# Performance work log

Measured on AMD Instinct MI355X. Metric: run time of the kernel, lower is better.

## Reference

```python
import jax, jax.numpy as jnp
import numpy as np
from jax import lax

N_FFT = 1024
HOP = 64
SR = 16000
N_MELS = 80
N_ITER = 300
N_FRAMES = 512
N_BINS = N_FFT // 2 + 1  # 513
SIG_LEN = N_FFT + HOP * (N_FRAMES - 1)  # 33728 (center=False istft length)

# periodic hann window (librosa default, sym=False)
_WIN_NP = (0.5 - 0.5 * np.cos(2.0 * np.pi * np.arange(N_FFT) / N_FFT)).astype(np.float32)
_WIN = jnp.asarray(_WIN_NP)
# frame gather indices for center=False framing: [N_FRAMES, N_FFT]
_FRAME_IDX_NP = np.arange(N_FRAMES)[:, None] * HOP + np.arange(N_FFT)[None, :]
_FRAME_IDX = jnp.asarray(_FRAME_IDX_NP)
# window-sum-squares normalization for istft overlap-add
_wss = np.zeros(SIG_LEN, np.float32)
np.add.at(_wss, _FRAME_IDX_NP, np.broadcast_to(_WIN_NP**2, (N_FRAMES, N_FFT)))
_WSS_SAFE = jnp.asarray(np.where(_wss > 1e-11, _wss, 1.0).astype(np.float32))


def _mel_filterbank(sr, n_fft, n_mels, fmin=0.0, fmax=None):
    """librosa.filters.mel with defaults: slaney mel scale, slaney norm."""
    if fmax is None:
        fmax = sr / 2.0
    f_sp = 200.0 / 3.0
    min_log_hz = 1000.0
    min_log_mel = min_log_hz / f_sp
    logstep = np.log(6.4) / 27.0

    def hz2mel(f):
        f = np.asarray(f, dtype=np.float64)
        return np.where(f >= min_log_hz,
                        min_log_mel + np.log(np.maximum(f, min_log_hz) / min_log_hz) / logstep,
                        f / f_sp)

    def mel2hz(m):
        m = np.asarray(m, dtype=np.float64)
        return np.where(m >= min_log_mel,
                        min_log_hz * np.exp(logstep * (m - min_log_mel)),
                        m * f_sp)

    mel_f = mel2hz(np.linspace(hz2mel(fmin), hz2mel(fmax), n_mels + 2))
    fft_f = np.linspace(0.0, sr / 2.0, 1 + n_fft // 2)
    fdiff = np.diff(mel_f)
    ramps = mel_f[:, None] - fft_f[None, :]
    lower = -ramps[:-2] / fdiff[:-1, None]
    upper = ramps[2:] / fdiff[1:, None]
    weights = np.maximum(0.0, np.minimum(lower, upper))
    enorm = 2.0 / (mel_f[2:n_mels + 2] - mel_f[:n_mels])  # slaney norm
    weights *= enorm[:, None]
    return weights.astype(np.float32)  # [n_mels, n_bins]


def _stft(x):
    # x: [SIG_LEN] -> [N_BINS, N_FRAMES], center=False, hann window
    frames = x[_FRAME_IDX] * _WIN  # [N_FRAMES, N_FFT]
    return jnp.fft.rfft(frames, axis=-1).T


def _istft(S):
    # S: [N_BINS, N_FRAMES] -> [SIG_LEN], center=False, hann window, NOLA norm
    frames = jnp.fft.irfft(S.T, n=N_FFT, axis=-1) * _WIN  # [N_FRAMES, N_FFT]
    ola = jnp.zeros(SIG_LEN, dtype=frames.dtype).at[_FRAME_IDX].add(frames)
    return ola / _WSS_SAFE


def setup_inputs() -> dict:
    key = jax.random.key(0)
    mel = jax.random.normal(key, (N_MELS, N_FRAMES), dtype=jnp.float32)
    basis = _mel_filterbank(SR, N_FFT, N_MELS)           # [80, 513]
    inv_mel_basis = np.linalg.pinv(basis).astype(np.float32)  # [513, 80]
    return {"mel": mel, "inv_mel_basis": jnp.asarray(inv_mel_basis)}


def reference(mel, inv_mel_basis):
    # mel -> linear magnitude via pseudo-inverse mel basis
    mag = inv_mel_basis @ jnp.power(10.0, mel)  # [N_BINS, N_FRAMES]

    def step(X_best, _):
        x_t = _istft(X_best)
        est = _stft(x_t)
        phase = est / jnp.maximum(1e-8, jnp.abs(est))
        return (mag * phase).astype(jnp.complex64), None

    X0 = mag.astype(jnp.complex64)
    X_final, _ = lax.scan(step, X0, None, length=N_ITER)
    return jnp.real(_istft(X_final))  # [SIG_LEN]
```

## Files before the change

kernel.cpp:

```cpp
#include <hip/hip_runtime.h>
#include <math.h>

#define NFFT   1024
#define NH     512
#define HOP    64
#define NMELS  80
#define NFR    512
#define NBINS  513
#define NITER  300
#define SIGLEN 33728
#define NSEG   527
#define NT     256
#define NB     512

#define TBL_WIN  0
#define TBL_TWR  1024
#define TBL_TWI  1280
#define TBL_W1R  1536
#define TBL_W1I  2056
#define BAR_SLOT 2624
#define BAR_GEN  3200
#define OFF_MAG  4096
#define OFF_IWS  266752
#define OFF_F    300480
#define OFF_X    824768

typedef unsigned long long u64;
typedef unsigned int u32;

__device__ __forceinline__ float4 coh_load4(const float* p) {
    u64 a = __hip_atomic_load((const u64*)p,       __ATOMIC_RELAXED, __HIP_MEMORY_SCOPE_AGENT);
    u64 b = __hip_atomic_load((const u64*)(p + 2), __ATOMIC_RELAXED, __HIP_MEMORY_SCOPE_AGENT);
    float2 fa, fb;
    __builtin_memcpy(&fa, &a, 8);
    __builtin_memcpy(&fb, &b, 8);
    return make_float4(fa.x, fa.y, fb.x, fb.y);
}
__device__ __forceinline__ void coh_store4(float* p, float4 v) {
    float2 fa = make_float2(v.x, v.y), fb = make_float2(v.z, v.w);
    u64 a, b;
    __builtin_memcpy(&a, &fa, 8);
    __builtin_memcpy(&b, &fb, 8);
    __hip_atomic_store((u64*)p,       a, __ATOMIC_RELAXED, __HIP_MEMORY_SCOPE_AGENT);
    __hip_atomic_store((u64*)(p + 2), b, __ATOMIC_RELAXED, __HIP_MEMORY_SCOPE_AGENT);
}
__device__ __forceinline__ float coh_load1(const float* p) {
    u32 a = __hip_atomic_load((const u32*)p, __ATOMIC_RELAXED, __HIP_MEMORY_SCOPE_AGENT);
    float f;
    __builtin_memcpy(&f, &a, 4);
    return f;
}
__device__ __forceinline__ void coh_store1(float* p, float v) {
    u32 a;
    __builtin_memcpy(&a, &v, 4);
    __hip_atomic_store((u32*)p, a, __ATOMIC_RELAXED, __HIP_MEMORY_SCOPE_AGENT);
}

template<int P, int SH, bool INV>
__device__ __forceinline__ void r4b(const float* __restrict__ sR, const float* __restrict__ sI,
                                    float* __restrict__ dR, float* __restrict__ dI,
                                    const float* twr, const float* twi, int j) {
    int k  = j & (P - 1);
    int d0 = ((j - k) << 2) + k;
    float x0r = sR[j],       x0i = sI[j];
    float x1r = sR[j + 128], x1i = sI[j + 128];
    float x2r = sR[j + 256], x2i = sI[j + 256];
    float x3r = sR[j + 384], x3i = sI[j + 384];
    int tb = k << SH;
    float c1 = twr[tb], s1 = twi[tb];
    if (INV) s1 = -s1;
    float c2 = c1 * c1 - s1 * s1, s2 = 2.f * c1 * s1;
    float c3 = c1 * c2 - s1 * s2, s3 = c1 * s2 + s1 * c2;
    float a1r = x1r * c1 - x1i * s1, a1i = x1r * s1 + x1i * c1;
    float a2r = x2r * c2 - x2i * s2, a2i = x2r * s2 + x2i * c2;
    float a3r = x3r * c3 - x3i * s3, a3i = x3r * s3 + x3i * c3;
    float t0r = x0r + a2r, t0i = x0i + a2i;
    float t1r = x0r - a2r, t1i = x0i - a2i;
    float t2r = a1r + a3r, t2i = a1i + a3i;
    float t3r = a1r - a3r, t3i = a1i - a3i;
    float i3r = INV ? -t3i : t3i;
    float i3i = INV ?  t3r : -t3r;
    dR[d0]         = t0r + t2r;  dI[d0]         = t0i + t2i;
    dR[d0 + P]     = t1r + i3r;  dI[d0 + P]     = t1i + i3i;
    dR[d0 + 2 * P] = t0r - t2r;  dI[d0 + 2 * P] = t0i - t2i;
    dR[d0 + 3 * P] = t1r - i3r;  dI[d0 + 3 * P] = t1i - i3i;
}

struct __align__(16) SMemI {
    float xb[NFFT];
    float C0r[NH], C0i[NH];
    float C1r[NH], C1i[NH];
    float win[NFFT];
    float twr[256], twi[256];
    float mag[516];
};

extern "C" __global__ __launch_bounds__(NT)
void k_init(const float* __restrict__ mel,
            const float* __restrict__ invmel,
            float* __restrict__ ws) {
    __shared__ SMemI sm;
    const int tid = threadIdx.x;
    const int t   = blockIdx.x;

    for (int n = tid; n < NFFT; n += NT) {
        double a = (2.0 * 3.14159265358979323846) * (double)n / 1024.0;
        sm.win[n] = (float)(0.5 - 0.5 * cos(a));
    }
    for (int j = tid; j < 256; j += NT) {
        double a = (2.0 * 3.14159265358979323846) * (double)j / 512.0;
        sm.twr[j] = (float)cos(a);
        sm.twi[j] = (float)(-sin(a));
    }
    __syncthreads();
    if (t == 0) {
        for (int n = tid; n < NFFT; n += NT) ws[TBL_WIN + n] = sm.win[n];
        for (int j = tid; j < 256; j += NT) {
            ws[TBL_TWR + j] = sm.twr[j];
            ws[TBL_TWI + j] = sm.twi[j];
        }
        for (int k = tid; k < NBINS; k += NT) {
            double a = (2.0 * 3.14159265358979323846) * (double)k / 1024.0;
            ws[TBL_W1R + k] = (float)cos(a);
            ws[TBL_W1I + k] = (float)sin(a);
        }
        ((int*)ws)[BAR_SLOT + tid]       = 0;
        ((int*)ws)[BAR_SLOT + 256 + tid] = 0;
        if (tid == 0) ((int*)ws)[BAR_GEN] = 0;
    }

    for (int p = t * NT + tid; p < SIGLEN; p += NFR * NT) {
        int tq = p >> 6, io = p & 63;
        float s = 0.f;
#pragma unroll
        for (int m = 0; m < 16; ++m) {
            int tp = tq - m;
            if (tp >= 0 && tp < NFR) {
                float w = sm.win[io + (m << 6)];
                s += w * w;
            }
        }
        ws[OFF_IWS + p] = (s > 1e-11f) ? (1.0f / s) : 1.0f;
    }

    if (tid < NMELS) sm.xb[tid] = exp10f(mel[tid * NFR + t]);
    __syncthreads();
    for (int k = tid; k < NBINS; k += NT) {
        const float* row = invmel + k * NMELS;
        float s = 0.f;
#pragma unroll 8
        for (int j = 0; j < NMELS; ++j) s += row[j] * sm.xb[j];
        ws[OFF_MAG + t * NBINS + k] = s;
        sm.mag[k] = s;
    }
    __syncthreads();

    for (int k = tid; k < NH; k += NT) {
        float xr = sm.mag[k], yr = sm.mag[512 - k];
        double a = (2.0 * 3.14159265358979323846) * (double)k / 1024.0;
        float c = (float)cos(a), s = (float)sin(a);
        float dr = xr - yr;
        sm.C1r[k] = ((xr + yr) - s * dr) * (1.0f / 1024.0f);
        sm.C1i[k] = (c * dr) * (1.0f / 1024.0f);
    }
    __syncthreads();
    if (tid < 128) {
        float x0r = sm.C1r[tid],       x0i = sm.C1i[tid];
        float x1r = sm.C1r[tid + 128], x1i = sm.C1i[tid + 128];
        float x2r = sm.C1r[tid + 256], x2i = sm.C1i[tid + 256];
        float x3r = sm.C1r[tid + 384], x3i = sm.C1i[tid + 384];
        float t0r = x0r + x2r, t0i = x0i + x2i;
        float t1r = x0r - x2r, t1i = x0i - x2i;
        float t2r = x1r + x3r, t2i = x1i + x3i;
        float t3r = x1r - x3r, t3i = x1i - x3i;
        float4 vr = make_float4(t0r + t2r, t1r - t3i, t0r - t2r, t1r + t3i);
        float4 vi = make_float4(t0i + t2i, t1i + t3r, t0i - t2i, t1i - t3r);
        ((float4*)sm.C0r)[tid] = vr;
        ((float4*)sm.C0i)[tid] = vi;
    }
    __syncthreads();
    if (tid < 128) r4b<4, 5, true>(sm.C0r, sm.C0i, sm.C1r, sm.C1i, sm.twr, sm.twi, tid);
    __syncthreads();
    if (tid < 128) r4b<16, 3, true>(sm.C1r, sm.C1i, sm.C0r, sm.C0i, sm.twr, sm.twi, tid);
    __syncthreads();
    if (tid < 128) r4b<64, 1, true>(sm.C0r, sm.C0i, sm.C1r, sm.C1i, sm.twr, sm.twi, tid);
    __syncthreads();
    {
        float c = sm.twr[tid], s = -sm.twi[tid];
        float x0r = sm.C1r[tid], x0i = sm.C1i[tid];
        float x1r = sm.C1r[tid + 256], x1i = sm.C1i[tid + 256];
        float ar = x1r * c - x1i * s, ai = x1r * s + x1i * c;
        sm.C0r[tid]       = x0r + ar;  sm.C0i[tid]       = x0i + ai;
        sm.C0r[tid + 256] = x0r - ar;  sm.C0i[tid + 256] = x0i - ai;
    }
    __syncthreads();

    float4 w4 = ((float4*)sm.win)[tid];
    float4 o;
    o.x = w4.x * sm.C0r[2 * tid];
    o.y = w4.y * sm.C0i[2 * tid];
    o.z = w4.z * sm.C0r[2 * tid + 1];
    o.w = w4.w * sm.C0i[2 * tid + 1];
    *(float4*)&ws[OFF_F + (t << 10) + (tid << 2)] = o;
}

struct __align__(16) SM1 {
    float C0r[NH], C0i[NH];
    float C1r[NH], C1i[NH];
    float twr[256], twi[256];
};

__device__ __forceinline__ void gbar(int* bar, int t, int tid, int bc) {
    __syncthreads();
    if (tid == 0)
        __hip_atomic_store(bar + BAR_SLOT + t, bc,
                           __ATOMIC_RELAXED, __HIP_MEMORY_SCOPE_AGENT);
    if (t == 0) {
        while (__hip_atomic_load(bar + BAR_SLOT + tid,
                                 __ATOMIC_RELAXED, __HIP_MEMORY_SCOPE_AGENT) < bc)
            __builtin_amdgcn_s_sleep(1);
        while (__hip_atomic_load(bar + BAR_SLOT + 256 + tid,
                                 __ATOMIC_RELAXED, __HIP_MEMORY_SCOPE_AGENT) < bc)
            __builtin_amdgcn_s_sleep(1);
        __syncthreads();
        if (tid == 0)
            __hip_atomic_store(bar + BAR_GEN, bc,
                               __ATOMIC_RELAXED, __HIP_MEMORY_SCOPE_AGENT);
    }
    if (tid == 0) {
        while (__hip_atomic_load(bar + BAR_GEN,
                                 __ATOMIC_RELAXED, __HIP_MEMORY_SCOPE_AGENT) < bc)
            __builtin_amdgcn_s_sleep(2);
    }
    __syncthreads();
}

extern "C" __global__ __launch_bounds__(NT)
void k_persist(float* __restrict__ ws, float* __restrict__ out) {
    __shared__ SM1 sm;
    const int tid = threadIdx.x;
    const int t   = blockIdx.x;
    const int i0  = tid << 2;
    const int j2  = 512 - tid;
    const int n0  = tid << 1;

    const float* tbl  = ws;
    const float* magg = ws + OFF_MAG;
    const float* iws  = ws + OFF_IWS;
    float* F  = ws + OFF_F;
    float* X  = ws + OFF_X;
    int*   bar = (int*)ws;

    if (tid < 64)       ((float4*)sm.twr)[tid]      = ((const float4*)(tbl + TBL_TWR))[tid];
    else if (tid < 128) ((float4*)sm.twi)[tid - 64] = ((const float4*)(tbl + TBL_TWI))[tid - 64];

    float4 w4 = ((const float4*)(tbl + TBL_WIN))[tid];
    float m_a, m_b, m_ny = 0.f, w1r_a, w1i_a, w1r_b, w1i_b;
    {
        const int s0 = t * NBINS;
        if (tid == 0) {
            m_a = magg[s0]; m_ny = magg[s0 + 512]; m_b = magg[s0 + 256];
            w1r_a = 1.f; w1i_a = 0.f; w1r_b = 0.f; w1i_b = 1.f;
        } else {
            m_a = magg[s0 + tid]; m_b = magg[s0 + j2];
            w1r_a = tbl[TBL_W1R + tid]; w1i_a = tbl[TBL_W1I + tid];
            w1r_b = tbl[TBL_W1R + j2];  w1i_b = tbl[TBL_W1I + j2];
        }
    }
    const bool extra = (t >= 497);
    int gseg = -1;
    if (tid < 64) gseg = t;
    else if (tid < 128 && extra) gseg = t + 15;
    const int u = tid & 63;
    float iwreg = 0.f;
    if (gseg >= 0) iwreg = iws[(gseg << 6) + u];

    if (gseg >= 0) {
        float acc = 0.f;
#pragma unroll
        for (int m = 0; m < 16; ++m) {
            int tp = gseg - m;
            if (tp >= 0 && tp < NFR)
                acc += coh_load1(&F[(tp << 10) + u + (m << 6)]);
        }
        coh_store1(&X[(gseg << 6) + u], acc * iwreg);
    }
    gbar(bar, t, tid, 1);

    int bc = 2;
#pragma unroll 1
    for (int it = 1; it <= NITER; ++it) {
        {
            float4 xv = coh_load4(&X[(t << 6) + i0]);
            sm.C1r[n0]     = xv.x * w4.x;
            sm.C1i[n0]     = xv.y * w4.y;
            sm.C1r[n0 + 1] = xv.z * w4.z;
            sm.C1i[n0 + 1] = xv.w * w4.w;
        }
        __syncthreads();
        if (tid < 128) {
            float x0r = sm.C1r[tid],       x0i = sm.C1i[tid];
            float x1r = sm.C1r[tid + 128], x1i = sm.C1i[tid + 128];
            float x2r = sm.C1r[tid + 256], x2i = sm.C1i[tid + 256];
            float x3r = sm.C1r[tid + 384], x3i = sm.C1i[tid + 384];
            float t0r = x0r + x2r, t0i = x0i + x2i;
            float t1r = x0r - x2r, t1i = x0i - x2i;
            float t2r = x1r + x3r, t2i = x1i + x3i;
            float t3r = x1r - x3r, t3i = x1i - x3i;
            float4 vr = make_float4(t0r + t2r, t1r + t3i, t0r - t2r, t1r - t3i);
            float4 vi = make_float4(t0i + t2i, t1i - t3r, t0i - t2i, t1i + t3r);
            ((float4*)sm.C0r)[tid] = vr;
            ((float4*)sm.C0i)[tid] = vi;
        }
        __syncthreads();
        if (tid < 128) r4b<4, 5, false>(sm.C0r, sm.C0i, sm.C1r, sm.C1i, sm.twr, sm.twi, tid);
        __syncthreads();
        if (tid < 128) r4b<16, 3, false>(sm.C1r, sm.C1i, sm.C0r, sm.C0i, sm.twr, sm.twi, tid);
        __syncthreads();
        if (tid < 128) r4b<64, 1, false>(sm.C0r, sm.C0i, sm.C1r, sm.C1i, sm.twr, sm.twi, tid);
        __syncthreads();
        {
            float c = sm.twr[tid], s = sm.twi[tid];
            float x0r = sm.C1r[tid], x0i = sm.C1i[tid];
            float x1r = sm.C1r[tid + 256], x1i = sm.C1i[tid + 256];
            float ar = x1r * c - x1i * s, ai = x1r * s + x1i * c;
            sm.C0r[tid]       = x0r + ar;  sm.C0i[tid]       = x0i + ai;
            sm.C0r[tid + 256] = x0r - ar;  sm.C0i[tid + 256] = x0i - ai;
        }
        __syncthreads();

        if (tid == 0) {
            float zr = sm.C0r[0], zi = sm.C0i[0];
            float e0 = zr + zi;
            float e5 = zr - zi;
            float X0 = m_a  * e0 / fmaxf(1e-8f, fabsf(e0));
            float X5 = m_ny * e5 / fmaxf(1e-8f, fabsf(e5));
            sm.C1r[0] = (X0 + X5) * (1.0f / 1024.0f);
            sm.C1i[0] = (X0 - X5) * (1.0f / 1024.0f);
            float z6r = sm.C0r[256], z6i = sm.C0i[256];
            float sc6 = m_b / fmaxf(1e-8f, sqrtf(z6r * z6r + z6i * z6i));
            float X6r = z6r * sc6, X6i = -z6i * sc6;
            sm.C1r[256] = X6r * (2.0f / 1024.0f);
            sm.C1i[256] = -X6i * (2.0f / 1024.0f);
        } else {
            float zr = sm.C0r[tid], zi = sm.C0i[tid];
            float ur = sm.C0r[j2],  ui = sm.C0i[j2];
            float er = 0.5f * (zr + ur), ei = 0.5f * (zi - ui);
            float dr = zr - ur,          di = zi + ui;
            float odr = 0.5f * di, odi = -0.5f * dr;
            float e1r = er + w1r_a * odr + w1i_a * odi;
            float e1i = ei + w1r_a * odi - w1i_a * odr;
            float e2r =  er + w1r_b * odr - w1i_b * odi;
            float e2i = -ei - w1r_b * odi - w1i_b * odr;
            float sc1 = m_a / fmaxf(1e-8f, sqrtf(e1r * e1r + e1i * e1i));
            float sc2 = m_b / fmaxf(1e-8f, sqrtf(e2r * e2r + e2i * e2i));
            float X1r = e1r * sc1, X1i = e1i * sc1;
            float X2r = e2r * sc2, X2i = e2i * sc2;
            float Er = X1r + X2r, Ei = X1i - X2i;
            float Dr = X1r - X2r, Di = X1i + X2i;
            float wdr = w1r_a * Dr - w1i_a * Di, wdi = w1r_a * Di + w1i_a * Dr;
            sm.C1r[tid] = (Er - wdi) * (1.0f / 1024.0f);
            sm.C1i[tid] = (Ei + wdr) * (1.0f / 1024.0f);
            float wdr2 = -w1r_b * Dr - w1i_b * Di, wdi2 = w1r_b * Di - w1i_b * Dr;
            sm.C1r[j2] = (Er - wdi2) * (1.0f / 1024.0f);
            sm.C1i[j2] = (-Ei + wdr2) * (1.0f / 1024.0f);
        }
        __syncthreads();

        if (tid < 128) {
            float x0r = sm.C1r[tid],       x0i = sm.C1i[tid];
            float x1r = sm.C1r[tid + 128], x1i = sm.C1i[tid + 128];
            float x2r = sm.C1r[tid + 256], x2i = sm.C1i[tid + 256];
            float x3r = sm.C1r[tid + 384], x3i = sm.C1i[tid + 384];
            float t0r = x0r + x2r, t0i = x0i + x2i;
            float t1r = x0r - x2r, t1i = x0i - x2i;
            float t2r = x1r + x3r, t2i = x1i + x3i;
            float t3r = x1r - x3r, t3i = x1i - x3i;
            float4 vr = make_float4(t0r + t2r, t1r - t3i, t0r - t2r, t1r + t3i);
            float4 vi = make_float4(t0i + t2i, t1i + t3r, t0i - t2i, t1i - t3r);
            ((float4*)sm.C0r)[tid] = vr;
            ((float4*)sm.C0i)[tid] = vi;
        }
        __syncthreads();
        if (tid < 128) r4b<4, 5, true>(sm.C0r, sm.C0i, sm.C1r, sm.C1i, sm.twr, sm.twi, tid);
        __syncthreads();
        if (tid < 128) r4b<16, 3, true>(sm.C1r, sm.C1i, sm.C0r, sm.C0i, sm.twr, sm.twi, tid);
        __syncthreads();
        if (tid < 128) r4b<64, 1, true>(sm.C0r, sm.C0i, sm.C1r, sm.C1i, sm.twr, sm.twi, tid);
        __syncthreads();
        {
            float c = sm.twr[tid], s = -sm.twi[tid];
            float x0r = sm.C1r[tid], x0i = sm.C1i[tid];
            float x1r = sm.C1r[tid + 256], x1i = sm.C1i[tid + 256];
            float ar = x1r * c - x1i * s, ai = x1r * s + x1i * c;
            sm.C0r[tid]       = x0r + ar;  sm.C0i[tid]       = x0i + ai;
            sm.C0r[tid + 256] = x0r - ar;  sm.C0i[tid + 256] = x0i - ai;
        }
        __syncthreads();

        {
            float4 o;
            o.x = w4.x * sm.C0r[n0];
            o.y = w4.y * sm.C0i[n0];
            o.z = w4.z * sm.C0r[n0 + 1];
            o.w = w4.w * sm.C0i[n0 + 1];
            coh_store4(&F[(t << 10) + i0], o);
        }
        gbar(bar, t, tid, bc++);

        if (gseg >= 0) {
            float acc = 0.f;
#pragma unroll
            for (int m = 0; m < 16; ++m) {
                int tp = gseg - m;
                if (tp >= 0 && tp < NFR)
                    acc += coh_load1(&F[(tp << 10) + u + (m << 6)]);
            }
            float val = acc * iwreg;
            if (it < NITER) coh_store1(&X[(gseg << 6) + u], val);
            else            out[(gseg << 6) + u] = val;
        }
        if (it < NITER)
            gbar(bar, t, tid, bc++);
    }
}

extern "C" void kernel_launch(void* const* d_in, const int* in_sizes, int n_in,
                              void* d_out, int out_size, void* d_ws, size_t ws_size,
                              hipStream_t stream) {
    const float* mel    = (const float*)d_in[0];
    const float* invmel = (const float*)d_in[1];
    float* out = (float*)d_out;
    float* ws  = (float*)d_ws;

    k_init<<<NFR, NT, 0, stream>>>(mel, invmel, ws);
    k_persist<<<NB, NT, 0, stream>>>(ws, out);
}
```

Before: 3.108 ms.

## Shrink persistent blocks to a single wavefront and vectorize barrier polling

Each persistent block (one per frame) now runs one 64-lane wavefront instead of 256 threads. Every lane processes several FFT elements per stage, and window, magnitude and twiddle tables are staged in shared memory instead of registers. With one wave per block, __syncthreads becomes nearly free, and the grid barrier's master block polls 8 slots per lane across 64 lanes rather than 256 lanes in two passes. The aim is to cut intra-block and grid-barrier synchronisation cost in the 300-iteration loop. In exchange, each wave does four times the serial work per FFT stage, with more LDS traffic and fewer threads to hide latency.

```diff
diff --git a/kernel.cpp b/kernel.cpp
--- a/kernel.cpp
+++ b/kernel.cpp
@@ -9,8 +9,8 @@
 #define NBINS  513
 #define NITER  300
 #define SIGLEN 33728
-#define NSEG   527
-#define NT     256
+#define NTI    256
+#define NTW    64
 #define NB     512
 
 #define TBL_WIN  0
@@ -95,7 +95,7 @@
     float mag[516];
 };
 
-extern "C" __global__ __launch_bounds__(NT)
+extern "C" __global__ __launch_bounds__(NTI)
 void k_init(const float* __restrict__ mel,
             const float* __restrict__ invmel,
             float* __restrict__ ws) {
@@ -103,23 +103,23 @@
     const int tid = threadIdx.x;
     const int t   = blockIdx.x;
 
-    for (int n = tid; n < NFFT; n += NT) {
+    for (int n = tid; n < NFFT; n += NTI) {
         double a = (2.0 * 3.14159265358979323846) * (double)n / 1024.0;
         sm.win[n] = (float)(0.5 - 0.5 * cos(a));
     }
-    for (int j = tid; j < 256; j += NT) {
+    for (int j = tid; j < 256; j += NTI) {
         double a = (2.0 * 3.14159265358979323846) * (double)j / 512.0;
         sm.twr[j] = (float)cos(a);
         sm.twi[j] = (float)(-sin(a));
     }
     __syncthreads();
     if (t == 0) {
-        for (int n = tid; n < NFFT; n += NT) ws[TBL_WIN + n] = sm.win[n];
-        for (int j = tid; j < 256; j += NT) {
+        for (int n = tid; n < NFFT; n += NTI) ws[TBL_WIN + n] = sm.win[n];
+        for (int j = tid; j < 256; j += NTI) {
             ws[TBL_TWR + j] = sm.twr[j];
             ws[TBL_TWI + j] = sm.twi[j];
         }
-        for (int k = tid; k < NBINS; k += NT) {
+        for (int k = tid; k < NBINS; k += NTI) {
             double a = (2.0 * 3.14159265358979323846) * (double)k / 1024.0;
             ws[TBL_W1R + k] = (float)cos(a);
             ws[TBL_W1I + k] = (float)sin(a);
@@ -129,7 +129,7 @@
         if (tid == 0) ((int*)ws)[BAR_GEN] = 0;
     }
 
-    for (int p = t * NT + tid; p < SIGLEN; p += NFR * NT) {
+    for (int p = t * NTI + tid; p < SIGLEN; p += NFR * NTI) {
         int tq = p >> 6, io = p & 63;
         float s = 0.f;
 #pragma unroll
@@ -145,7 +145,7 @@
 
     if (tid < NMELS) sm.xb[tid] = exp10f(mel[tid * NFR + t]);
     __syncthreads();
-    for (int k = tid; k < NBINS; k += NT) {
+    for (int k = tid; k < NBINS; k += NTI) {
         const float* row = invmel + k * NMELS;
         float s = 0.f;
 #pragma unroll 8
@@ -155,7 +155,7 @@
     }
     __syncthreads();
 
-    for (int k = tid; k < NH; k += NT) {
+    for (int k = tid; k < NH; k += NTI) {
         float xr = sm.mag[k], yr = sm.mag[512 - k];
         double a = (2.0 * 3.14159265358979323846) * (double)k / 1024.0;
         float c = (float)cos(a), s = (float)sin(a);
@@ -204,30 +204,46 @@
     *(float4*)&ws[OFF_F + (t << 10) + (tid << 2)] = o;
 }
 
-struct __align__(16) SM1 {
+struct __align__(16) SMW {
     float C0r[NH], C0i[NH];
     float C1r[NH], C1i[NH];
     float twr[256], twi[256];
+    float win[NFFT];
+    float mag[520], w1r[520], w1i[520];
 };
 
-__device__ __forceinline__ void gbar(int* bar, int t, int tid, int bc) {
-    __syncthreads();
-    if (tid == 0)
+__device__ __forceinline__ void gbar(int* bar, int t, int l, int bc) {
+    __syncthreads();
+    if (l == 0)
         __hip_atomic_store(bar + BAR_SLOT + t, bc,
                            __ATOMIC_RELAXED, __HIP_MEMORY_SCOPE_AGENT);
     if (t == 0) {
-        while (__hip_atomic_load(bar + BAR_SLOT + tid,
-                                 __ATOMIC_RELAXED, __HIP_MEMORY_SCOPE_AGENT) < bc)
+        const int* base = bar + BAR_SLOT + (l << 3);
+        for (;;) {
+            int a0 = __hip_atomic_load(base + 0, __ATOMIC_RELAXED, __HIP_MEMORY_SCOPE_AGENT);
+            int a1 = __hip_atomic_load(base + 1, __ATOMIC_RELAXED, __HIP_MEMORY_SCOPE_AGENT);
+            int a2 = __hip_atomic_load(base + 2, __ATOMIC_RELAXED, __HIP_MEMORY_SCOPE_AGENT);
+            int a3 = __hip_atomic_load(base + 3, __ATOMIC_RELAXED, __HIP_MEMORY_SCOPE_AGENT);
+            int a4 = __hip_atomic_load(base + 4, __ATOMIC_RELAXED, __HIP_MEMORY_SCOPE_AGENT);
+            int a5 = __hip_atomic_load(base + 5, __ATOMIC_RELAXED, __HIP_MEMORY_SCOPE_AGENT);
+            int a6 = __hip_atomic_load(base + 6, __ATOMIC_RELAXED, __HIP_MEMORY_SCOPE_AGENT);
+            int a7 = __hip_atomic_load(base + 7, __ATOMIC_RELAXED, __HIP_MEMORY_SCOPE_AGENT);
+            int m01 = a0 < a1 ? a0 : a1;
+            int m23 = a2 < a3 ? a2 : a3;
+            int m45 = a4 < a5 ? a4 : a5;
+            int m67 = a6 < a7 ? a6 : a7;
+            int m03 = m01 < m23 ? m01 : m23;
+            int m47 = m45 < m67 ? m45 : m67;
+            int mn  = m03 < m47 ? m03 : m47;
+            if (mn >= bc) break;
             __builtin_amdgcn_s_sleep(1);
-        while (__hip_atomic_load(bar + BAR_SLOT + 256 + tid,
-                                 __ATOMIC_RELAXED, __HIP_MEMORY_SCOPE_AGENT) < bc)
-            __builtin_amdgcn_s_sleep(1);
-        __syncthreads();
-        if (tid == 0)
+        }
+        __syncthreads();
+        if (l == 0)
             __hip_atomic_store(bar + BAR_GEN, bc,
                                __ATOMIC_RELAXED, __HIP_MEMORY_SCOPE_AGENT);
     }
-    if (tid == 0) {
+    if (l == 0) {
         while (__hip_atomic_load(bar + BAR_GEN,
                                  __ATOMIC_RELAXED, __HIP_MEMORY_SCOPE_AGENT) < bc)
             __builtin_amdgcn_s_sleep(2);
@@ -235,14 +251,11 @@
     __syncthreads();
 }
 
-extern "C" __global__ __launch_bounds__(NT)
+extern "C" __global__ __launch_bounds__(NTW)
 void k_persist(float* __restrict__ ws, float* __restrict__ out) {
-    __shared__ SM1 sm;
-    const int tid = threadIdx.x;
-    const int t   = blockIdx.x;
-    const int i0  = tid << 2;
-    const int j2  = 512 - tid;
-    const int n0  = tid << 1;
+    __shared__ SMW sm;
+    const int l = threadIdx.x;
+    const int t = blockIdx.x;
 
     const float* tbl  = ws;
     const float* magg = ws + OFF_MAG;
@@ -251,177 +264,220 @@
     float* X  = ws + OFF_X;
     int*   bar = (int*)ws;
 
-    if (tid < 64)       ((float4*)sm.twr)[tid]      = ((const float4*)(tbl + TBL_TWR))[tid];
-    else if (tid < 128) ((float4*)sm.twi)[tid - 64] = ((const float4*)(tbl + TBL_TWI))[tid - 64];
-
-    float4 w4 = ((const float4*)(tbl + TBL_WIN))[tid];
-    float m_a, m_b, m_ny = 0.f, w1r_a, w1i_a, w1r_b, w1i_b;
+    ((float4*)sm.twr)[l] = ((const float4*)(tbl + TBL_TWR))[l];
+    ((float4*)sm.twi)[l] = ((const float4*)(tbl + TBL_TWI))[l];
+#pragma unroll
+    for (int c = 0; c < 4; ++c)
+        ((float4*)sm.win)[l + (c << 6)] = ((const float4*)(tbl + TBL_WIN))[l + (c << 6)];
+    for (int k = l; k < NBINS; k += NTW) {
+        sm.mag[k] = magg[t * NBINS + k];
+        sm.w1r[k] = tbl[TBL_W1R + k];
+        sm.w1i[k] = tbl[TBL_W1I + k];
+    }
+    const bool extra = (t >= 497);
+    float iw0 = iws[(t << 6) + l];
+    float iw1 = extra ? iws[((t + 15) << 6) + l] : 0.f;
+    __syncthreads();
+
     {
-        const int s0 = t * NBINS;
-        if (tid == 0) {
-            m_a = magg[s0]; m_ny = magg[s0 + 512]; m_b = magg[s0 + 256];
-            w1r_a = 1.f; w1i_a = 0.f; w1r_b = 0.f; w1i_b = 1.f;
-        } else {
-            m_a = magg[s0 + tid]; m_b = magg[s0 + j2];
-            w1r_a = tbl[TBL_W1R + tid]; w1i_a = tbl[TBL_W1I + tid];
-            w1r_b = tbl[TBL_W1R + j2];  w1i_b = tbl[TBL_W1I + j2];
-        }
-    }
-    const bool extra = (t >= 497);
-    int gseg = -1;
-    if (tid < 64) gseg = t;
-    else if (tid < 128 && extra) gseg = t + 15;
-    const int u = tid & 63;
-    float iwreg = 0.f;
-    if (gseg >= 0) iwreg = iws[(gseg << 6) + u];
-
-    if (gseg >= 0) {
         float acc = 0.f;
 #pragma unroll
         for (int m = 0; m < 16; ++m) {
-            int tp = gseg - m;
+            int tp = t - m;
             if (tp >= 0 && tp < NFR)
-                acc += coh_load1(&F[(tp << 10) + u + (m << 6)]);
-        }
-        coh_store1(&X[(gseg << 6) + u], acc * iwreg);
-    }
-    gbar(bar, t, tid, 1);
+                acc += coh_load1(&F[(tp << 10) + l + (m << 6)]);
+        }
+        coh_store1(&X[(t << 6) + l], acc * iw0);
+        if (extra) {
+            int g = t + 15;
+            float acc2 = 0.f;
+#pragma unroll
+            for (int m = 0; m < 16; ++m) {
+                int tp = g - m;
+                if (tp >= 0 && tp < NFR)
+                    acc2 += coh_load1(&F[(tp << 10) + l + (m << 6)]);
+            }
+            coh_store1(&X[(g << 6) + l], acc2 * iw1);
+        }
+    }
+    gbar(bar, t, l, 1);
 
     int bc = 2;
 #pragma unroll 1
     for (int it = 1; it <= NITER; ++it) {
-        {
+#pragma unroll
+        for (int c = 0; c < 4; ++c) {
+            int tp = l + (c << 6);
+            int i0 = tp << 2;
             float4 xv = coh_load4(&X[(t << 6) + i0]);
-            sm.C1r[n0]     = xv.x * w4.x;
-            sm.C1i[n0]     = xv.y * w4.y;
-            sm.C1r[n0 + 1] = xv.z * w4.z;
-            sm.C1i[n0 + 1] = xv.w * w4.w;
-        }
-        __syncthreads();
-        if (tid < 128) {
-            float x0r = sm.C1r[tid],       x0i = sm.C1i[tid];
-            float x1r = sm.C1r[tid + 128], x1i = sm.C1i[tid + 128];
-            float x2r = sm.C1r[tid + 256], x2i = sm.C1i[tid + 256];
-            float x3r = sm.C1r[tid + 384], x3i = sm.C1i[tid + 384];
+            float4 wv = ((float4*)sm.win)[tp];
+            int n0 = tp << 1;
+            sm.C1r[n0]     = xv.x * wv.x;
+            sm.C1i[n0]     = xv.y * wv.y;
+            sm.C1r[n0 + 1] = xv.z * wv.z;
+            sm.C1i[n0 + 1] = xv.w * wv.w;
+        }
+        __syncthreads();
+#pragma unroll
+        for (int c = 0; c < 2; ++c) {
+            int j = l + (c << 6);
+            float x0r = sm.C1r[j],       x0i = sm.C1i[j];
+            float x1r = sm.C1r[j + 128], x1i = sm.C1i[j + 128];
+            float x2r = sm.C1r[j + 256], x2i = sm.C1i[j + 256];
+            float x3r = sm.C1r[j + 384], x3i = sm.C1i[j + 384];
             float t0r = x0r + x2r, t0i = x0i + x2i;
             float t1r = x0r - x2r, t1i = x0i - x2i;
             float t2r = x1r + x3r, t2i = x1i + x3i;
             float t3r = x1r - x3r, t3i = x1i - x3i;
             float4 vr = make_float4(t0r + t2r, t1r + t3i, t0r - t2r, t1r - t3i);
             float4 vi = make_float4(t0i + t2i, t1i - t3r, t0i - t2i, t1i + t3r);
-            ((float4*)sm.C0r)[tid] = vr;
-            ((float4*)sm.C0i)[tid] = vi;
-        }
-        __syncthreads();
-        if (tid < 128) r4b<4, 5, false>(sm.C0r, sm.C0i, sm.C1r, sm.C1i, sm.twr, sm.twi, tid);
-        __syncthreads();
-        if (tid < 128) r4b<16, 3, false>(sm.C1r, sm.C1i, sm.C0r, sm.C0i, sm.twr, sm.twi, tid);
-        __syncthreads();
-        if (tid < 128) r4b<64, 1, false>(sm.C0r, sm.C0i, sm.C1r, sm.C1i, sm.twr, sm.twi, tid);
-        __syncthreads();
-        {
-            float c = sm.twr[tid], s = sm.twi[tid];
-            float x0r = sm.C1r[tid], x0i = sm.C1i[tid];
-            float x1r = sm.C1r[tid + 256], x1i = sm.C1i[tid + 256];
-            float ar = x1r * c - x1i * s, ai = x1r * s + x1i * c;
-            sm.C0r[tid]       = x0r + ar;  sm.C0i[tid]       = x0i + ai;
-            sm.C0r[tid + 256] = x0r - ar;  sm.C0i[tid + 256] = x0i - ai;
-        }
-        __syncthreads();
-
-        if (tid == 0) {
-            float zr = sm.C0r[0], zi = sm.C0i[0];
-            float e0 = zr + zi;
-            float e5 = zr - zi;
-            float X0 = m_a  * e0 / fmaxf(1e-8f, fabsf(e0));
-            float X5 = m_ny * e5 / fmaxf(1e-8f, fabsf(e5));
-            sm.C1r[0] = (X0 + X5) * (1.0f / 1024.0f);
-            sm.C1i[0] = (X0 - X5) * (1.0f / 1024.0f);
-            float z6r = sm.C0r[256], z6i = sm.C0i[256];
-            float sc6 = m_b / fmaxf(1e-8f, sqrtf(z6r * z6r + z6i * z6i));
-            float X6r = z6r * sc6, X6i = -z6i * sc6;
-            sm.C1r[256] = X6r * (2.0f / 1024.0f);
-            sm.C1i[256] = -X6i * (2.0f / 1024.0f);
-        } else {
-            float zr = sm.C0r[tid], zi = sm.C0i[tid];
-            float ur = sm.C0r[j2],  ui = sm.C0i[j2];
-            float er = 0.5f * (zr + ur), ei = 0.5f * (zi - ui);
-            float dr = zr - ur,          di = zi + ui;
-            float odr = 0.5f * di, odi = -0.5f * dr;
-            float e1r = er + w1r_a * odr + w1i_a * odi;
-            float e1i = ei + w1r_a * odi - w1i_a * odr;
-            float e2r =  er + w1r_b * odr - w1i_b * odi;
-            float e2i = -ei - w1r_b * odi - w1i_b * odr;
-            float sc1 = m_a / fmaxf(1e-8f, sqrtf(e1r * e1r + e1i * e1i));
-            float sc2 = m_b / fmaxf(1e-8f, sqrtf(e2r * e2r + e2i * e2i));
-            float X1r = e1r * sc1, X1i = e1i * sc1;
-            float X2r = e2r * sc2, X2i = e2i * sc2;
-            float Er = X1r + X2r, Ei = X1i - X2i;
-            float Dr = X1r - X2r, Di = X1i + X2i;
-            float wdr = w1r_a * Dr - w1i_a * Di, wdi = w1r_a * Di + w1i_a * Dr;
-            sm.C1r[tid] = (Er - wdi) * (1.0f / 1024.0f);
-            sm.C1i[tid] = (Ei + wdr) * (1.0f / 1024.0f);
-            float wdr2 = -w1r_b * Dr - w1i_b * Di, wdi2 = w1r_b * Di - w1i_b * Dr;
-            sm.C1r[j2] = (Er - wdi2) * (1.0f / 1024.0f);
-            sm.C1i[j2] = (-Ei + wdr2) * (1.0f / 1024.0f);
-        }
-        __syncthreads();
-
-        if (tid < 128) {
-            float x0r = sm.C1r[tid],       x0i = sm.C1i[tid];
-            float x1r = sm.C1r[tid + 128], x1i = sm.C1i[tid + 128];
-            float x2r = sm.C1r[tid + 256], x2i = sm.C1i[tid + 256];
-            float x3r = sm.C1r[tid + 384], x3i = sm.C1i[tid + 384];
+            ((float4*)sm.C0r)[j] = vr;
+            ((float4*)sm.C0i)[j] = vi;
+        }
+        __syncthreads();
+        r4b<4, 5, false>(sm.C0r, sm.C0i, sm.C1r, sm.C1i, sm.twr, sm.twi, l);
+        r4b<4, 5, false>(sm.C0r, sm.C0i, sm.C1r, sm.C1i, sm.twr, sm.twi, l + 64);
+        __syncthreads();
+        r4b<16, 3, false>(sm.C1r, sm.C1i, sm.C0r, sm.C0i, sm.twr, sm.twi, l);
+        r4b<16, 3, false>(sm.C1r, sm.C1i, sm.C0r, sm.C0i, sm.twr, sm.twi, l + 64);
+        __syncthreads();
+        r4b<64, 1, false>(sm.C0r, sm.C0i, sm.C1r, sm.C1i, sm.twr, sm.twi, l);
+        r4b<64, 1, false>(sm.C0r, sm.C0i, sm.C1r, sm.C1i, sm.twr, sm.twi, l + 64);
+        __syncthreads();
+#pragma unroll
+        for (int c = 0; c < 4; ++c) {
+            int tp = l + (c << 6);
+            float cc = sm.twr[tp], s = sm.twi[tp];
+            float x0r = sm.C1r[tp], x0i = sm.C1i[tp];
+            float x1r = sm.C1r[tp + 256], x1i = sm.C1i[tp + 256];
+            float ar = x1r * cc - x1i * s, ai = x1r * s + x1i * cc;
+            sm.C0r[tp]       = x0r + ar;  sm.C0i[tp]       = x0i + ai;
+            sm.C0r[tp + 256] = x0r - ar;  sm.C0i[tp + 256] = x0i - ai;
+        }
+        __syncthreads();
+#pragma unroll
+        for (int c = 0; c < 4; ++c) {
+            int tp = l + (c << 6);
+            if (tp == 0) {
+                float zr = sm.C0r[0], zi = sm.C0i[0];
+                float e0 = zr + zi;
+                float e5 = zr - zi;
+                float X0 = sm.mag[0]   * e0 / fmaxf(1e-8f, fabsf(e0));
+                float X5 = sm.mag[512] * e5 / fmaxf(1e-8f, fabsf(e5));
+                sm.C1r[0] = (X0 + X5) * (1.0f / 1024.0f);
+                sm.C1i[0] = (X0 - X5) * (1.0f / 1024.0f);
+                float z6r = sm.C0r[256], z6i = sm.C0i[256];
+                float sc6 = sm.mag[256] / fmaxf(1e-8f, sqrtf(z6r * z6r + z6i * z6i));
+                float X6r = z6r * sc6, X6i = -z6i * sc6;
+                sm.C1r[256] = X6r * (2.0f / 1024.0f);
+                sm.C1i[256] = -X6i * (2.0f / 1024.0f);
+            } else {
+                int j2 = 512 - tp;
+                float m_a = sm.mag[tp], m_b = sm.mag[j2];
+                float w1r_a = sm.w1r[tp], w1i_a = sm.w1i[tp];
+                float w1r_b = sm.w1r[j2], w1i_b = sm.w1i[j2];
+                float zr = sm.C0r[tp], zi = sm.C0i[tp];
+                float ur = sm.C0r[j2], ui = sm.C0i[j2];
+                float er = 0.5f * (zr + ur), ei = 0.5f * (zi - ui);
+                float dr = zr - ur,          di = zi + ui;
+                float odr = 0.5f * di, odi = -0.5f * dr;
+                float e1r = er + w1r_a * odr + w1i_a * odi;
+                float e1i = ei + w1r_a * odi - w1i_a * odr;
+                float e2r =  er + w1r_b * odr - w1i_b * odi;
+                float e2i = -ei - w1r_b * odi - w1i_b * odr;
+                float sc1 = m_a / fmaxf(1e-8f, sqrtf(e1r * e1r + e1i * e1i));
+                float sc2 = m_b / fmaxf(1e-8f, sqrtf(e2r * e2r + e2i * e2i));
+                float X1r = e1r * sc1, X1i = e1i * sc1;
+                float X2r = e2r * sc2, X2i = e2i * sc2;
+                float Er = X1r + X2r, Ei = X1i - X2i;
+                float Dr = X1r - X2r, Di = X1i + X2i;
+                float wdr = w1r_a * Dr - w1i_a * Di, wdi = w1r_a * Di + w1i_a * Dr;
+                sm.C1r[tp] = (Er - wdi) * (1.0f / 1024.0f);
+                sm.C1i[tp] = (Ei + wdr) * (1.0f / 1024.0f);
+                float wdr2 = -w1r_b * Dr - w1i_b * Di, wdi2 = w1r_b * Di - w1i_b * Dr;
+                sm.C1r[j2] = (Er - wdi2) * (1.0f / 1024.0f);
+                sm.C1i[j2] = (-Ei + wdr2) * (1.0f / 1024.0f);
+            }
+        }
+        __syncthreads();
+#pragma unroll
+        for (int c = 0; c < 2; ++c) {
+            int j = l + (c << 6);
+            float x0r = sm.C1r[j],       x0i = sm.C1i[j];
+            float x1r = sm.C1r[j + 128], x1i = sm.C1i[j + 128];
+            float x2r = sm.C1r[j + 256], x2i = sm.C1i[j + 256];
+            float x3r = sm.C1r[j + 384], x3i = sm.C1i[j + 384];
             float t0r = x0r + x2r, t0i = x0i + x2i;
             float t1r = x0r - x2r, t1i = x0i - x2i;
             float t2r = x1r + x3r, t2i = x1i + x3i;
             float t3r = x1r - x3r, t3i = x1i - x3i;
             float4 vr = make_float4(t0r + t2r, t1r - t3i, t0r - t2r, t1r + t3i);
             float4 vi = make_float4(t0i + t2i, t1i + t3r, t0i - t2i, t1i - t3r);
-            ((float4*)sm.C0r)[tid] = vr;
-            ((float4*)sm.C0i)[tid] = vi;
-        }
-        __syncthreads();
-        if (tid < 128) r4b<4, 5, true>(sm.C0r, sm.C0i, sm.C1r, sm.C1i, sm.twr, sm.twi, tid);
-        __syncthreads();
-        if (tid < 128) r4b<16, 3, true>(sm.C1r, sm.C1i, sm.C0r, sm.C0i, sm.twr, sm.twi, tid);
-        __syncthreads();
-        if (tid < 128) r4b<64, 1, true>(sm.C0r, sm.C0i, sm.C1r, sm.C1i, sm.twr, sm.twi, tid);
-        __syncthreads();
+            ((float4*)sm.C0r)[j] = vr;
+            ((float4*)sm.C0i)[j] = vi;
+        }
+        __syncthreads();
+        r4b<4, 5, true>(sm.C0r, sm.C0i, sm.C1r, sm.C1i, sm.twr, sm.twi, l);
+        r4b<4, 5, true>(sm.C0r, sm.C0i, sm.C1r, sm.C1i, sm.twr, sm.twi, l + 64);
+        __syncthreads();
+        r4b<16, 3, true>(sm.C1r, sm.C1i, sm.C0r, sm.C0i, sm.twr, sm.twi, l);
+        r4b<16, 3, true>(sm.C1r, sm.C1i, sm.C0r, sm.C0i, sm.twr, sm.twi, l + 64);
+        __syncthreads();
+        r4b<64, 1, true>(sm.C0r, sm.C0i, sm.C1r, sm.C1i, sm.twr, sm.twi, l);
+        r4b<64, 1, true>(sm.C0r, sm.C0i, sm.C1r, sm.C1i, sm.twr, sm.twi, l + 64);
+        __syncthreads();
+#pragma unroll
+        for (int c = 0; c < 4; ++c) {
+            int tp = l + (c << 6);
+            float cc = sm.twr[tp], s = -sm.twi[tp];
+            float x0r = sm.C1r[tp], x0i = sm.C1i[tp];
+            float x1r = sm.C1r[tp + 256], x1i = sm.C1i[tp + 256];
+            float ar = x1r * cc - x1i * s, ai = x1r * s + x1i * cc;
+            sm.C0r[tp]       = x0r + ar;  sm.C0i[tp]       = x0i + ai;
+            sm.C0r[tp + 256] = x0r - ar;  sm.C0i[tp + 256] = x0i - ai;
+        }
+        __syncthreads();
+#pragma unroll
+        for (int c = 0; c < 4; ++c) {
+            int tp = l + (c << 6);
+            int i0 = tp << 2, n0 = tp << 1;
+            float4 wv = ((float4*)sm.win)[tp];
+            float4 o;
+            o.x = wv.x * sm.C0r[n0];
+            o.y = wv.y * sm.C0i[n0];
+            o.z = wv.z * sm.C0r[n0 + 1];
+            o.w = wv.w * sm.C0i[n0 + 1];
+            coh_store4(&F[(t << 10) + i0], o);
+        }
+        gbar(bar, t, l, bc++);
+
         {
-            float c = sm.twr[tid], s = -sm.twi[tid];
-            float x0r = sm.C1r[tid], x0i = sm.C1i[tid];
-            float x1r = sm.C1r[tid + 256], x1i = sm.C1i[tid + 256];
-            float ar = x1r * c - x1i * s, ai = x1r * s + x1i * c;
-            sm.C0r[tid]       = x0r + ar;  sm.C0i[tid]       = x0i + ai;
-            sm.C0r[tid + 256] = x0r - ar;  sm.C0i[tid + 256] = x0i - ai;
-        }
-        __syncthreads();
-
-        {
-            float4 o;
-            o.x = w4.x * sm.C0r[n0];
-            o.y = w4.y * sm.C0i[n0];
-            o.z = w4.z * sm.C0r[n0 + 1];
-            o.w = w4.w * sm.C0i[n0 + 1];
-            coh_store4(&F[(t << 10) + i0], o);
-        }
-        gbar(bar, t, tid, bc++);
-
-        if (gseg >= 0) {
             float acc = 0.f;
 #pragma unroll
             for (int m = 0; m < 16; ++m) {
-                int tp = gseg - m;
+                int tp = t - m;
                 if (tp >= 0 && tp < NFR)
-                    acc += coh_load1(&F[(tp << 10) + u + (m << 6)]);
+                    acc += coh_load1(&F[(tp << 10) + l + (m << 6)]);
             }
-            float val = acc * iwreg;
-            if (it < NITER) coh_store1(&X[(gseg << 6) + u], val);
-            else            out[(gseg << 6) + u] = val;
+            float val = acc * iw0;
+            if (it < NITER) coh_store1(&X[(t << 6) + l], val);
+            else            out[(t << 6) + l] = val;
+            if (extra) {
+                int g = t + 15;
+                float acc2 = 0.f;
+#pragma unroll
+                for (int m = 0; m < 16; ++m) {
+                    int tp = g - m;
+                    if (tp >= 0 && tp < NFR)
+                        acc2 += coh_load1(&F[(tp << 10) + l + (m << 6)]);
+                }
+                float val2 = acc2 * iw1;
+                if (it < NITER) coh_store1(&X[(g << 6) + l], val2);
+                else            out[(g << 6) + l] = val2;
+            }
         }
         if (it < NITER)
-            gbar(bar, t, tid, bc++);
+            gbar(bar, t, l, bc++);
     }
 }
 
@@ -433,6 +489,6 @@
     float* out = (float*)d_out;
     float* ws  = (float*)d_ws;
 
-    k_init<<<NFR, NT, 0, stream>>>(mel, invmel, ws);
-    k_persist<<<NB, NT, 0, stream>>>(ws, out);
-}
+    k_init<<<NFR, NTI, 0, stream>>>(mel, invmel, ws);
+    k_persist<<<NB, NTW, 0, stream>>>(ws, out);
+}
```

Measured after the change: 4.635 ms. +49.1%, slower.
